# Optimization experiments

Measured on AMD Instinct MI355X. Metric: run time of the kernel, lower is better.

## Reference

```python
import jax, jax.numpy as jnp
import numpy as np

N = 100000   # nodes
E = 1600000  # edges
D_IN, D_H, D_OUT = 128, 128, 64
BN_EPS = 1e-5


def setup_inputs() -> dict:
    key = jax.random.key(0)
    ks = jax.random.split(key, 12)

    def lin_w(k, fan_in, shape):
        s = 1.0 / np.sqrt(fan_in)
        return jax.random.uniform(k, shape, jnp.float32, -s, s)

    return {
        "x": jax.random.normal(ks[0], (N, D_IN), jnp.float32),
        "edge_index": jax.random.randint(ks[1], (2, E), 0, N, dtype=jnp.int64),
        "edge_weight": jax.random.uniform(ks[2], (E,), jnp.float32),
        "W1": lin_w(ks[3], D_IN, (D_IN, D_H)),
        "b1": jnp.zeros((D_H,), jnp.float32),
        "W2": lin_w(ks[4], D_H, (D_H, D_H)),
        "b2": jnp.zeros((D_H,), jnp.float32),
        "W3": lin_w(ks[5], D_H, (D_H, D_OUT)),
        "b3": jnp.zeros((D_OUT,), jnp.float32),
        "gamma1": jnp.ones((D_H,), jnp.float32),
        "beta1": jnp.zeros((D_H,), jnp.float32),
        "gamma2": jnp.ones((D_H,), jnp.float32),
        "beta2": jnp.zeros((D_H,), jnp.float32),
    }


def _gcn_conv(x, src, dst, w, W, b):
    # PyG GCNConv: x' = D^{-1/2} (A + I) D^{-1/2} (x W) + b, self-loop weight 1
    n = x.shape[0]
    h = x @ W                                   # [N, d_out]
    loop = jnp.arange(n, dtype=src.dtype)
    s = jnp.concatenate([src, loop])            # [E+N]
    d = jnp.concatenate([dst, loop])
    ww = jnp.concatenate([w, jnp.ones((n,), w.dtype)])
    deg = jax.ops.segment_sum(ww, d, num_segments=n)          # in-degree at targets
    dinv = jnp.where(deg > 0, jax.lax.rsqrt(deg), 0.0)
    norm = dinv[s] * ww * dinv[d]               # [E+N]
    msg = h[s] * norm[:, None]                  # gather + scale
    out = jax.ops.segment_sum(msg, d, num_segments=n)
    return out + b


def _batch_norm(x, gamma, beta):
    mean = jnp.mean(x, axis=0)
    var = jnp.mean(jnp.square(x - mean), axis=0)  # biased, as BatchNorm uses
    return (x - mean) * jax.lax.rsqrt(var + BN_EPS) * gamma + beta


def reference(x, edge_index, edge_weight, W1, b1, W2, b2, W3, b3,
              gamma1, beta1, gamma2, beta2):
    src, dst = edge_index[0], edge_index[1]
    h = _gcn_conv(x, src, dst, edge_weight, W1, b1)
    h = jax.nn.relu(_batch_norm(h, gamma1, beta1))
    h = _gcn_conv(h, src, dst, edge_weight, W2, b2)
    h = jax.nn.relu(_batch_norm(h, gamma2, beta2))
    return _gcn_conv(h, src, dst, edge_weight, W3, b3)
```

## Files before the change

kernel.cpp:

```cpp
#include <hip/hip_runtime.h>
#include <hip/hip_fp16.h>
#include <cstdint>
#include <cstddef>

#define BN_EPS 1e-5f
#define KB 256
#define BSH 9

typedef _Float16 half8 __attribute__((ext_vector_type(8)));
typedef float floatx4 __attribute__((ext_vector_type(4)));

__device__ __forceinline__ float loadS(const __half* p) { return __half2float(*p); }
__device__ __forceinline__ float2 load2(const __half* p) {
    return __half22float2(*(const __half2*)p);
}
__device__ __forceinline__ void storeS(float* p, float v) { *p = v; }
__device__ __forceinline__ void storeS(__half* p, float v) { *p = __float2half(v); }
__device__ __forceinline__ void store2(float* p, float a, float b) {
    *(float2*)p = make_float2(a, b);
}
__device__ __forceinline__ void store2(__half* p, float a, float b) {
    *(__half2*)p = __floats2half2_rn(a, b);
}
__device__ __forceinline__ float wn_of(unsigned v) {
    __half_raw hr; hr.x = (unsigned short)(v & 0x7fffu);
    return __half2float((__half)hr);
}

static __device__ __forceinline__ int load_edge(const void* ei, int mode64, long long pos) {
    if (mode64) return (int)((const long long*)ei)[pos];
    return ((const int*)ei)[pos];
}

__device__ __forceinline__ int detect_mode64(const unsigned* eiw) {
    const int lane = (int)threadIdx.x & 63;
    unsigned m = 0;
    for (int i = lane; i < 2048; i += 64) m |= eiw[2 * i + 1];
    return (__ballot(m != 0) == 0ULL) ? 1 : 0;
}

__global__ __launch_bounds__(256) void init_hist_kernel(const void* __restrict__ ei,
                                                        unsigned* __restrict__ tk,
                                                        unsigned* __restrict__ pc, int E, int epb,
                                                        const float* __restrict__ W1,
                                                        const float* __restrict__ W2,
                                                        const float* __restrict__ W3,
                                                        _Float16* __restrict__ WT1,
                                                        _Float16* __restrict__ WT2,
                                                        _Float16* __restrict__ WT3) {
    const int bid = (int)blockIdx.x;
    const int tid = (int)threadIdx.x;
    if (bid < 160) {
        if (bid == 0 && tid < 8) tk[tid] = 0u;
        const int t_ = bid;
        if (t_ < 64) {
            int t = t_ * 256 + tid;
            int n = t / 128, k = t % 128;
            WT1[t] = (_Float16)W1[k * 128 + n];
        } else if (t_ < 128) {
            int t = (t_ - 64) * 256 + tid;
            int n = t / 128, k = t % 128;
            WT2[t] = (_Float16)W2[k * 128 + n];
        } else {
            int t = (t_ - 128) * 256 + tid;
            int n = t / 128, k = t % 128;
            WT3[t] = (_Float16)W3[k * 64 + n];
        }
        return;
    }
    __shared__ unsigned h[256];
    const int k = bid - 160;
    h[tid] = 0;
    __syncthreads();
    const int md = detect_mode64((const unsigned*)ei);
    const int e0 = k * epb;
    const int e1 = min(E, e0 + epb);
    for (int e = e0 + tid; e < e1; e += 256) {
        int d = load_edge(ei, md, (long long)E + e);
        atomicAdd(&h[d >> BSH], 1u);
    }
    __syncthreads();
    pc[k * 256 + tid] = h[tid];
}

__global__ __launch_bounds__(256) void scan_pc_kernel(unsigned* __restrict__ pc,
                                                      int* __restrict__ tb,
                                                      int* __restrict__ bbase,
                                                      float* __restrict__ gsum,
                                                      float* __restrict__ gsq,
                                                      unsigned* __restrict__ tk, int nbuck) {
    __shared__ int red[256];
    __shared__ int lastFlag;
    const int b = (int)blockIdx.x;
    const int tid = (int)threadIdx.x;
    const unsigned v = pc[tid * 256 + b];
    red[tid] = (int)v;
    __syncthreads();
    for (int off = 1; off < 256; off <<= 1) {
        int t = 0;
        if (tid >= off) t = red[tid - off];
        __syncthreads();
        red[tid] += t;
        __syncthreads();
    }
    pc[tid * 256 + b] = (unsigned)(red[tid] - (int)v);
    if (tid == 255)
        __hip_atomic_store(&tb[b], red[255], __ATOMIC_RELEASE, __HIP_MEMORY_SCOPE_AGENT);
    __syncthreads();
    if (tid == 0) {
        unsigned t = __hip_atomic_fetch_add(tk, 1u, __ATOMIC_ACQ_REL, __HIP_MEMORY_SCOPE_AGENT);
        lastFlag = (t == (unsigned)gridDim.x - 1u) ? 1 : 0;
    }
    __syncthreads();
    if (!lastFlag) return;
    const int v2 = (tid < nbuck)
        ? __hip_atomic_load(&tb[tid], __ATOMIC_ACQUIRE, __HIP_MEMORY_SCOPE_AGENT) : 0;
    __syncthreads();
    red[tid] = v2;
    __syncthreads();
    for (int off = 1; off < 256; off <<= 1) {
        int t = 0;
        if (tid >= off) t = red[tid - off];
        __syncthreads();
        red[tid] += t;
        __syncthreads();
    }
    bbase[tid] = red[tid] - v2;
    if (tid < 128) { gsum[tid] = 0.0f; gsq[tid] = 0.0f; }
}

template <int M, bool BN, typename TI, bool SCALE>
__device__ __forceinline__ void gemm_body(int gbid, const TI* __restrict__ X,
                                          const _Float16* __restrict__ WTg,
                                          const float* __restrict__ sc,
                                          const float* __restrict__ sh,
                                          const float* __restrict__ dinvp,
                                          __half* __restrict__ Hout, int N,
                                          _Float16* WT ) {
    constexpr int CT = M / 16;
    constexpr int LDK = 136;

    for (int t = threadIdx.x; t < M * 16; t += 256) {
        int n = t / 16, seg = t % 16;
        *(half8*)&WT[n * LDK + seg * 8] = *(const half8*)&WTg[n * 128 + seg * 8];
    }
    __syncthreads();

    const int wave = (int)threadIdx.x >> 6;
    const int lane = (int)threadIdx.x & 63;
    const int qd = lane >> 4;
    const int ln = lane & 15;
    const int tile0 = gbid * 64 + wave * 16;
    int ar = tile0 + ln;
    if (ar >= N) ar = N - 1;

    half8 aF[4];
    const TI* xr = X + (size_t)ar * 128 + qd * 8;
#pragma unroll
    for (int kb = 0; kb < 4; ++kb) {
        float vv[8];
        if constexpr (sizeof(TI) == 4) {
            float4 v0 = *(const float4*)(xr + kb * 32);
            float4 v1 = *(const float4*)(xr + kb * 32 + 4);
            vv[0] = v0.x; vv[1] = v0.y; vv[2] = v0.z; vv[3] = v0.w;
            vv[4] = v1.x; vv[5] = v1.y; vv[6] = v1.z; vv[7] = v1.w;
        } else {
            half8 raw = *(const half8*)(xr + kb * 32);
#pragma unroll
            for (int j = 0; j < 8; ++j) vv[j] = (float)raw[j];
        }
        if (BN) {
            const int kbase = kb * 32 + qd * 8;
#pragma unroll
            for (int j = 0; j < 8; ++j)
                vv[j] = fmaxf(fmaf(vv[j], sc[kbase + j], sh[kbase + j]), 0.0f);
        }
        half8 a;
#pragma unroll
        for (int j = 0; j < 8; ++j) a[j] = (_Float16)vv[j];
        aF[kb] = a;
    }

    float dvr[4];
    if constexpr (SCALE) {
#pragma unroll
        for (int r = 0; r < 4; ++r) {
            int orow = tile0 + qd * 4 + r;
            dvr[r] = (orow < N) ? dinvp[orow] : 1.0f;
        }
    }

#pragma unroll
    for (int ct = 0; ct < CT; ++ct) {
        floatx4 acc = {0.0f, 0.0f, 0.0f, 0.0f};
#pragma unroll
        for (int kb = 0; kb < 4; ++kb) {
            half8 b = *(const half8*)&WT[(ct * 16 + ln) * LDK + kb * 32 + qd * 8];
            acc = __builtin_amdgcn_mfma_f32_16x16x32_f16(aF[kb], b, acc, 0, 0, 0);
        }
#pragma unroll
        for (int r = 0; r < 4; ++r) {
            int orow = tile0 + qd * 4 + r;
            if (orow < N) {
                float o = acc[r];
                if constexpr (SCALE) o *= dvr[r];
                Hout[(size_t)orow * M + ct * 16 + ln] = __float2half(o);
            }
        }
    }
}

__global__ __launch_bounds__(256) void sort_gemm1_kernel(const void* __restrict__ ei,
                                                         const float* __restrict__ ew,
                                                         const unsigned* __restrict__ pc,
                                                         const int* __restrict__ bbase,
                                                         unsigned long long* __restrict__ sortedE,
                                                         int E, int epb, int GB,
                                                         const float* __restrict__ X,
                                                         const _Float16* __restrict__ WT1g,
                                                         __half* __restrict__ Hout, int N) {
    __shared__ _Float16 WT[128 * 136];
    __shared__ unsigned off_s[256];
    if ((int)blockIdx.x < GB) {
        gemm_body<128, false, float, false>(blockIdx.x, X, WT1g, nullptr, nullptr, nullptr,
                                            Hout, N, WT);
        return;
    }
    const int k = (int)blockIdx.x - GB;
    const int tid = (int)threadIdx.x;
    off_s[tid] = (unsigned)bbase[tid] + pc[k * 256 + tid];
    __syncthreads();
    const int md = detect_mode64((const unsigned*)ei);
    const int e0 = k * epb;
    const int e1 = min(E, e0 + epb);
    for (int e = e0 + tid; e < e1; e += 256) {
        int d = load_edge(ei, md, (long long)E + e);
        int s = load_edge(ei, md, e);
        float wv = ew[e];
        unsigned slot = atomicAdd(&off_s[d >> BSH], 1u);
        sortedE[slot] = ((unsigned long long)(unsigned)d << 33) |
                        ((unsigned long long)(unsigned)s << 16) |
                        (unsigned long long)(unsigned short)__half_as_ushort(__float2half(wv));
    }
}

__global__ __launch_bounds__(256) void csr_build_kernel(const unsigned long long* __restrict__ sortedE,
                                                        const int* __restrict__ bbase,
                                                        const int* __restrict__ tb,
                                                        float* __restrict__ dinv,
                                                        int* __restrict__ cnt,
                                                        int* __restrict__ row_start,
                                                        unsigned* __restrict__ edata,
                                                        __half* __restrict__ H, int N) {
    __shared__ unsigned cs[512];
    __shared__ float ws[512];
    __shared__ float dv[512];
    __shared__ unsigned sc[512];
    __shared__ unsigned cur[512];
    __shared__ int red[256];
    const int b = (int)blockIdx.x;
    const int tid = (int)threadIdx.x;
    const int n0 = b << BSH;
    const int base = bbase[b];
    const int len = tb[b];

    cs[tid] = 0; cs[tid + 256] = 0;
    ws[tid] = 0.0f; ws[tid + 256] = 0.0f;
    cur[tid] = 0; cur[tid + 256] = 0;
    __syncthreads();

    for (int i = tid; i < len; i += 256) {
        unsigned long long p = sortedE[base + i];
        unsigned fine = (unsigned)(p >> 33) - (unsigned)n0;
        atomicAdd(&cs[fine], 1u);
        __half_raw hr; hr.x = (unsigned short)(p & 0xFFFFu);
        atomicAdd(&ws[fine], __half2float((__half)hr));
    }
    __syncthreads();

    const unsigned a0 = cs[2 * tid];
    const unsigned a1 = cs[2 * tid + 1];
    const int s2 = (int)(a0 + a1);
    red[tid] = s2;
    __syncthreads();
    for (int off = 1; off < 256; off <<= 1) {
        int t = 0;
        if (tid >= off) t = red[tid - off];
        __syncthreads();
        red[tid] += t;
        __syncthreads();
    }
    const int excl2 = red[tid] - s2;
    sc[2 * tid] = (unsigned)excl2;
    sc[2 * tid + 1] = (unsigned)(excl2 + (int)a0);

#pragma unroll
    for (int q = 0; q < 2; ++q) {
        const int f = tid + q * 256;
        const int node = n0 + f;
        const float dvv = rsqrtf(1.0f + ws[f]);
        dv[f] = dvv;
        if (node < N) {
            dinv[node] = dvv;
            cnt[node] = (int)cs[f];
            row_start[node] = base + (int)sc[f];
        }
    }
    __syncthreads();

    for (int i = tid; i < len; i += 256) {
        unsigned long long p = sortedE[base + i];
        unsigned fine = (unsigned)(p >> 33) - (unsigned)n0;
        unsigned s = (unsigned)(p >> 16) & 0x1FFFFu;
        __half_raw hr; hr.x = (unsigned short)(p & 0xFFFFu);
        float wnp = __half2float((__half)hr) * dv[fine];
        unsigned r = atomicAdd(&cur[fine], 1u);
        unsigned hb = (unsigned)__half_as_ushort(__float2half(wnp)) & 0x7fffu;
        edata[base + (int)sc[fine] + (int)r] = (s << 15) | hb;
    }

    for (int idx = tid; idx < (1 << BSH) * 16; idx += 256) {
        const int r = idx >> 4;
        const int node = n0 + r;
        if (node < N) {
            const int seg = idx & 15;
            _Float16* hp = (_Float16*)H + (size_t)node * 128 + seg * 8;
            half8 h = *(half8*)hp;
            const float dvv = dv[r];
#pragma unroll
            for (int j = 0; j < 8; ++j) h[j] = (_Float16)((float)h[j] * dvv);
            *(half8*)hp = h;
        }
    }
}

template <int D, bool BIAS, typename TY>
__global__ __launch_bounds__(256) void agg_kernel(const __half* __restrict__ H,
                                                  const unsigned* __restrict__ edata,
                                                  const int* __restrict__ row_start,
                                                  const int* __restrict__ cnt,
                                                  const float* __restrict__ dinv,
                                                  const float* __restrict__ bias,
                                                  TY* __restrict__ Y, int N) {
    constexpr int VPT = D / 64;
    const int lane = (int)threadIdx.x & 63;
    const int i = (int)blockIdx.x * 4 + ((int)threadIdx.x >> 6);
    if (i >= N) return;
    const int c0 = lane * VPT;
    const float di = dinv[i];

    float acc0, acc1 = 0.0f;
    if constexpr (VPT == 2) {
        float2 h = load2(H + (size_t)i * D + c0);
        acc0 = di * h.x;
        acc1 = di * h.y;
    } else {
        acc0 = di * loadS(H + (size_t)i * D + c0);
    }

    const int base = row_start[i];
    const int n = cnt[i];
    for (int off = 0; off < n; off += 64) {
        const int rem = n - off;
        unsigned ev = 0;
        if (lane < rem) ev = edata[base + off + lane];
        const int mm = min(64, rem);
        for (int j = 0; j < mm; j += 8) {
            const unsigned e0 = __shfl(ev, j),     e1 = __shfl(ev, j + 1);
            const unsigned e2 = __shfl(ev, j + 2), e3 = __shfl(ev, j + 3);
            const unsigned e4 = __shfl(ev, j + 4), e5 = __shfl(ev, j + 5);
            const unsigned e6 = __shfl(ev, j + 6), e7 = __shfl(ev, j + 7);
            const float w0 = wn_of(e0), w1 = wn_of(e1), w2 = wn_of(e2), w3 = wn_of(e3);
            const float w4 = wn_of(e4), w5 = wn_of(e5), w6 = wn_of(e6), w7 = wn_of(e7);
            if constexpr (VPT == 2) {
                float2 h0 = load2(H + (size_t)(e0 >> 15) * D + c0);
                float2 h1 = load2(H + (size_t)(e1 >> 15) * D + c0);
                float2 h2 = load2(H + (size_t)(e2 >> 15) * D + c0);
                float2 h3 = load2(H + (size_t)(e3 >> 15) * D + c0);
                float2 h4 = load2(H + (size_t)(e4 >> 15) * D + c0);
                float2 h5 = load2(H + (size_t)(e5 >> 15) * D + c0);
                float2 h6 = load2(H + (size_t)(e6 >> 15) * D + c0);
                float2 h7 = load2(H + (size_t)(e7 >> 15) * D + c0);
                acc0 = fmaf(w0, h0.x, acc0); acc1 = fmaf(w0, h0.y, acc1);
                acc0 = fmaf(w1, h1.x, acc0); acc1 = fmaf(w1, h1.y, acc1);
                acc0 = fmaf(w2, h2.x, acc0); acc1 = fmaf(w2, h2.y, acc1);
                acc0 = fmaf(w3, h3.x, acc0); acc1 = fmaf(w3, h3.y, acc1);
                acc0 = fmaf(w4, h4.x, acc0); acc1 = fmaf(w4, h4.y, acc1);
                acc0 = fmaf(w5, h5.x, acc0); acc1 = fmaf(w5, h5.y, acc1);
                acc0 = fmaf(w6, h6.x, acc0); acc1 = fmaf(w6, h6.y, acc1);
                acc0 = fmaf(w7, h7.x, acc0); acc1 = fmaf(w7, h7.y, acc1);
            } else {
                float h0 = loadS(H + (size_t)(e0 >> 15) * D + c0);
                float h1 = loadS(H + (size_t)(e1 >> 15) * D + c0);
                float h2 = loadS(H + (size_t)(e2 >> 15) * D + c0);
                float h3 = loadS(H + (size_t)(e3 >> 15) * D + c0);
                float h4 = loadS(H + (size_t)(e4 >> 15) * D + c0);
                float h5 = loadS(H + (size_t)(e5 >> 15) * D + c0);
                float h6 = loadS(H + (size_t)(e6 >> 15) * D + c0);
                float h7 = loadS(H + (size_t)(e7 >> 15) * D + c0);
                acc0 = fmaf(w0, h0, acc0);
                acc0 = fmaf(w1, h1, acc0);
                acc0 = fmaf(w2, h2, acc0);
                acc0 = fmaf(w3, h3, acc0);
                acc0 = fmaf(w4, h4, acc0);
                acc0 = fmaf(w5, h5, acc0);
                acc0 = fmaf(w6, h6, acc0);
                acc0 = fmaf(w7, h7, acc0);
            }
        }
    }

    if constexpr (VPT == 2) {
        if (BIAS) { acc0 += bias[c0]; acc1 += bias[c0 + 1]; }
        store2(Y + (size_t)i * D + c0, acc0, acc1);
    } else {
        if (BIAS) acc0 += bias[c0];
        storeS(Y + (size_t)i * D + c0, acc0);
    }
}

template <int M, bool BN, typename TI, bool ZERO, bool SCALE>
__global__ __launch_bounds__(256) void gemm_mfma_kernel(const TI* __restrict__ X,
                                                        const _Float16* __restrict__ WTg,
                                                        const float* __restrict__ sc,
                                                        const float* __restrict__ sh,
                                                        const float* __restrict__ dinvp,
                                                        __half* __restrict__ Hout, int N,
                                                        float* __restrict__ gsum,
                                                        float* __restrict__ gsq, int GB) {
    __shared__ _Float16 WT[M * 136];
    if (ZERO && (int)blockIdx.x == GB) {
        if (threadIdx.x < 128) { gsum[threadIdx.x] = 0.0f; gsq[threadIdx.x] = 0.0f; }
        return;
    }
    gemm_body<M, BN, TI, SCALE>(blockIdx.x, X, WTg, sc, sh, dinvp, Hout, N, WT);
}

__global__ __launch_bounds__(256) void stats_kernel(const __half* __restrict__ Y,
                                                    float* __restrict__ gsum,
                                                    float* __restrict__ gsq,
                                                    unsigned* __restrict__ tk,
                                                    const float* __restrict__ gamma,
                                                    const float* __restrict__ beta,
                                                    float* __restrict__ sc,
                                                    float* __restrict__ sh, int N) {
    __shared__ float ls[256], lq[256];
    __shared__ int lastFlag;
    const int tid = (int)threadIdx.x;
    const int c = tid & 127;
    const int half_ = tid >> 7;
    float s = 0.0f, q = 0.0f;
    for (int row = (int)blockIdx.x * 2 + half_; row < N; row += 512) {
        float v = __half2float(Y[(size_t)row * 128 + c]);
        s += v;
        q = fmaf(v, v, q);
    }
    ls[tid] = s; lq[tid] = q;
    __syncthreads();
    if (tid < 128) {
        atomicAdd(&gsum[c], ls[tid] + ls[tid + 128]);
        atomicAdd(&gsq[c],  lq[tid] + lq[tid + 128]);
    }
    __syncthreads();
    if (tid == 0) {
        unsigned t = __hip_atomic_fetch_add(tk, 1u, __ATOMIC_ACQ_REL, __HIP_MEMORY_SCOPE_AGENT);
        lastFlag = (t == (unsigned)gridDim.x - 1u) ? 1 : 0;
    }
    __syncthreads();
    if (!lastFlag) return;
    if (tid < 128) {
        float gs = __hip_atomic_load(&gsum[tid], __ATOMIC_ACQUIRE, __HIP_MEMORY_SCOPE_AGENT);
        float gq = __hip_atomic_load(&gsq[tid], __ATOMIC_ACQUIRE, __HIP_MEMORY_SCOPE_AGENT);
        float inv_n = 1.0f / (float)N;
        float mean = gs * inv_n;
        float var = gq * inv_n - mean * mean;
        float scale = gamma[tid] * rsqrtf(var + BN_EPS);
        sc[tid] = scale;
        sh[tid] = beta[tid] - mean * scale;
    }
}

extern "C" void kernel_launch(void* const* d_in, const int* in_sizes, int n_in,
                              void* d_out, int out_size, void* d_ws, size_t ws_size,
                              hipStream_t stream) {
    const float* x   = (const float*)d_in[0];
    const void*  ei  = d_in[1];
    const float* ew  = (const float*)d_in[2];
    const float* W1  = (const float*)d_in[3];
    const float* W2  = (const float*)d_in[5];
    const float* W3  = (const float*)d_in[7];
    const float* b3  = (const float*)d_in[8];
    const float* g1  = (const float*)d_in[9];
    const float* be1 = (const float*)d_in[10];
    const float* g2  = (const float*)d_in[11];
    const float* be2 = (const float*)d_in[12];
    float* out = (float*)d_out;

    const int N = in_sizes[0] / 128;
    const int E = in_sizes[2];

    char* w = (char*)d_ws;
    size_t off = 0;
    auto alloc = [&](size_t bytes) -> void* {
        void* p = w + off;
        off += (bytes + 255) & ~(size_t)255;
        return p;
    };
    unsigned* pc     = (unsigned*)alloc(256 * 256 * 4);
    int*   tb        = (int*)  alloc(256 * 4);
    int*   bbase     = (int*)  alloc(256 * 4);
    unsigned long long* sortedE = (unsigned long long*)alloc((size_t)E * 8);
    float* dinv      = (float*)alloc((size_t)N * 4);
    int*   cnt       = (int*)  alloc((size_t)N * 4);
    int*   row_start = (int*)  alloc((size_t)N * 4);
    unsigned* edata  = (unsigned*)alloc((size_t)E * 4);
    unsigned* tk     = (unsigned*)alloc(256);
    float* gsum      = (float*)alloc(128 * 4);
    float* gsq       = (float*)alloc(128 * 4);
    float* scb       = (float*)alloc(128 * 4);
    float* shb       = (float*)alloc(128 * 4);
    _Float16* WT1    = (_Float16*)alloc(128 * 128 * 2);
    _Float16* WT2    = (_Float16*)alloc(128 * 128 * 2);
    _Float16* WT3    = (_Float16*)alloc(128 * 64 * 2);
    __half* H        = (__half*)alloc((size_t)N * 128 * 2);
    __half* Yh       = (__half*)alloc((size_t)N * 128 * 2);
    (void)ws_size; (void)n_in; (void)out_size;

    const int epb   = (E + KB - 1) / KB;
    const int nbuck = (N + (1 << BSH) - 1) >> BSH;
    const int gb    = (N + 63) / 64;
    const int ab    = (N + 3) / 4;

    init_hist_kernel<<<160 + KB, 256, 0, stream>>>(ei, tk, pc, E, epb,
                                                   W1, W2, W3, WT1, WT2, WT3);
    scan_pc_kernel<<<nbuck, 256, 0, stream>>>(pc, tb, bbase, gsum, gsq, &tk[0], nbuck);
    sort_gemm1_kernel<<<gb + KB, 256, 0, stream>>>(ei, ew, pc, bbase, sortedE, E,
                                                   epb, gb, x, WT1, H, N);
    csr_build_kernel<<<nbuck, 256, 0, stream>>>(sortedE, bbase, tb, dinv, cnt, row_start,
                                                edata, H, N);

    agg_kernel<128, false, __half><<<ab, 256, 0, stream>>>(H, edata, row_start, cnt, dinv, nullptr, Yh, N);
    stats_kernel<<<256, 256, 0, stream>>>(Yh, gsum, gsq, &tk[1], g1, be1, scb, shb, N);

    gemm_mfma_kernel<128, true, __half, true, true><<<gb + 1, 256, 0, stream>>>(
        Yh, WT2, scb, shb, dinv, H, N, gsum, gsq, gb);
    agg_kernel<128, false, __half><<<ab, 256, 0, stream>>>(H, edata, row_start, cnt, dinv, nullptr, Yh, N);
    stats_kernel<<<256, 256, 0, stream>>>(Yh, gsum, gsq, &tk[2], g2, be2, scb, shb, N);

    gemm_mfma_kernel<64, true, __half, false, true><<<gb, 256, 0, stream>>>(
        Yh, WT3, scb, shb, dinv, H, N, nullptr, nullptr, gb);
    agg_kernel<64, true, float><<<ab, 256, 0, stream>>>(H, edata, row_start, cnt, dinv, b3, out, N);
}
```

Measured before the change: 513.2 us.

## Move source-side dinv scaling into aggregation and raise sort block count

Removes the pre-scaling of H rows by dinv from the GEMM epilogues and from the H rescale pass in csr_build. Instead, the aggregation kernel multiplies each edge weight by dinv of the source node, and the self term by dinv squared. This eliminates a read-modify-write pass over H and lets the GEMM1 blocks run independently of the CSR build. The costs are an extra random gather of dinv per edge in every aggregation and a larger count of histogram/sort blocks (KB from 256 to 1024), with the scan now summing four partitions per thread. The sort blocks are also reordered ahead of the GEMM blocks in the fused launch.

```diff
diff --git a/kernel.cpp b/kernel.cpp
--- a/kernel.cpp
+++ b/kernel.cpp
@@ -4,7 +4,7 @@
 #include <cstddef>
 
 #define BN_EPS 1e-5f
-#define KB 256
+#define KB 1024
 #define BSH 9
 
 typedef _Float16 half8 __attribute__((ext_vector_type(8)));
@@ -93,8 +93,16 @@
     __shared__ int lastFlag;
     const int b = (int)blockIdx.x;
     const int tid = (int)threadIdx.x;
-    const unsigned v = pc[tid * 256 + b];
-    red[tid] = (int)v;
+    unsigned v[4];
+    int vals[4];
+    int s = 0;
+#pragma unroll
+    for (int j = 0; j < 4; ++j) {
+        v[j] = pc[(tid * 4 + j) * 256 + b];
+        vals[j] = s;
+        s += (int)v[j];
+    }
+    red[tid] = s;
     __syncthreads();
     for (int off = 1; off < 256; off <<= 1) {
         int t = 0;
@@ -103,7 +111,10 @@
         red[tid] += t;
         __syncthreads();
     }
-    pc[tid * 256 + b] = (unsigned)(red[tid] - (int)v);
+    const int excl = red[tid] - s;
+#pragma unroll
+    for (int j = 0; j < 4; ++j)
+        pc[(tid * 4 + j) * 256 + b] = (unsigned)(excl + vals[j]);
     if (tid == 255)
         __hip_atomic_store(&tb[b], red[255], __ATOMIC_RELEASE, __HIP_MEMORY_SCOPE_AGENT);
     __syncthreads();
@@ -129,12 +140,11 @@
     if (tid < 128) { gsum[tid] = 0.0f; gsq[tid] = 0.0f; }
 }
 
-template <int M, bool BN, typename TI, bool SCALE>
+template <int M, bool BN, typename TI>
 __device__ __forceinline__ void gemm_body(int gbid, const TI* __restrict__ X,
                                           const _Float16* __restrict__ WTg,
                                           const float* __restrict__ sc,
                                           const float* __restrict__ sh,
-                                          const float* __restrict__ dinvp,
                                           __half* __restrict__ Hout, int N,
                                           _Float16* WT ) {
     constexpr int CT = M / 16;
@@ -181,15 +191,6 @@
         aF[kb] = a;
     }
 
-    float dvr[4];
-    if constexpr (SCALE) {
-#pragma unroll
-        for (int r = 0; r < 4; ++r) {
-            int orow = tile0 + qd * 4 + r;
-            dvr[r] = (orow < N) ? dinvp[orow] : 1.0f;
-        }
-    }
-
 #pragma unroll
     for (int ct = 0; ct < CT; ++ct) {
         floatx4 acc = {0.0f, 0.0f, 0.0f, 0.0f};
@@ -201,11 +202,7 @@
 #pragma unroll
         for (int r = 0; r < 4; ++r) {
             int orow = tile0 + qd * 4 + r;
-            if (orow < N) {
-                float o = acc[r];
-                if constexpr (SCALE) o *= dvr[r];
-                Hout[(size_t)orow * M + ct * 16 + ln] = __float2half(o);
-            }
+            if (orow < N) Hout[(size_t)orow * M + ct * 16 + ln] = __float2half(acc[r]);
         }
     }
 }
@@ -215,18 +212,18 @@
                                                          const unsigned* __restrict__ pc,
                                                          const int* __restrict__ bbase,
                                                          unsigned long long* __restrict__ sortedE,
-                                                         int E, int epb, int GB,
+                                                         int E, int epb,
                                                          const float* __restrict__ X,
                                                          const _Float16* __restrict__ WT1g,
                                                          __half* __restrict__ Hout, int N) {
     __shared__ _Float16 WT[128 * 136];
     __shared__ unsigned off_s[256];
-    if ((int)blockIdx.x < GB) {
-        gemm_body<128, false, float, false>(blockIdx.x, X, WT1g, nullptr, nullptr, nullptr,
-                                            Hout, N, WT);
+    if ((int)blockIdx.x >= KB) {
+        gemm_body<128, false, float>((int)blockIdx.x - KB, X, WT1g, nullptr, nullptr,
+                                     Hout, N, WT);
         return;
     }
-    const int k = (int)blockIdx.x - GB;
+    const int k = (int)blockIdx.x;
     const int tid = (int)threadIdx.x;
     off_s[tid] = (unsigned)bbase[tid] + pc[k * 256 + tid];
     __syncthreads();
@@ -250,8 +247,7 @@
                                                         float* __restrict__ dinv,
                                                         int* __restrict__ cnt,
                                                         int* __restrict__ row_start,
-                                                        unsigned* __restrict__ edata,
-                                                        __half* __restrict__ H, int N) {
+                                                        unsigned* __restrict__ edata, int N) {
     __shared__ unsigned cs[512];
     __shared__ float ws[512];
     __shared__ float dv[512];
@@ -317,20 +313,6 @@
         unsigned r = atomicAdd(&cur[fine], 1u);
         unsigned hb = (unsigned)__half_as_ushort(__float2half(wnp)) & 0x7fffu;
         edata[base + (int)sc[fine] + (int)r] = (s << 15) | hb;
-    }
-
-    for (int idx = tid; idx < (1 << BSH) * 16; idx += 256) {
-        const int r = idx >> 4;
-        const int node = n0 + r;
-        if (node < N) {
-            const int seg = idx & 15;
-            _Float16* hp = (_Float16*)H + (size_t)node * 128 + seg * 8;
-            half8 h = *(half8*)hp;
-            const float dvv = dv[r];
-#pragma unroll
-            for (int j = 0; j < 8; ++j) h[j] = (_Float16)((float)h[j] * dvv);
-            *(half8*)hp = h;
-        }
     }
 }
 
@@ -348,14 +330,15 @@
     if (i >= N) return;
     const int c0 = lane * VPT;
     const float di = dinv[i];
+    const float dii = di * di;
 
     float acc0, acc1 = 0.0f;
     if constexpr (VPT == 2) {
         float2 h = load2(H + (size_t)i * D + c0);
-        acc0 = di * h.x;
-        acc1 = di * h.y;
+        acc0 = dii * h.x;
+        acc1 = dii * h.y;
     } else {
-        acc0 = di * loadS(H + (size_t)i * D + c0);
+        acc0 = dii * loadS(H + (size_t)i * D + c0);
     }
 
     const int base = row_start[i];
@@ -370,8 +353,14 @@
             const unsigned e2 = __shfl(ev, j + 2), e3 = __shfl(ev, j + 3);
             const unsigned e4 = __shfl(ev, j + 4), e5 = __shfl(ev, j + 5);
             const unsigned e6 = __shfl(ev, j + 6), e7 = __shfl(ev, j + 7);
-            const float w0 = wn_of(e0), w1 = wn_of(e1), w2 = wn_of(e2), w3 = wn_of(e3);
-            const float w4 = wn_of(e4), w5 = wn_of(e5), w6 = wn_of(e6), w7 = wn_of(e7);
+            const float w0 = dinv[e0 >> 15] * wn_of(e0);
+            const float w1 = dinv[e1 >> 15] * wn_of(e1);
+            const float w2 = dinv[e2 >> 15] * wn_of(e2);
+            const float w3 = dinv[e3 >> 15] * wn_of(e3);
+            const float w4 = dinv[e4 >> 15] * wn_of(e4);
+            const float w5 = dinv[e5 >> 15] * wn_of(e5);
+            const float w6 = dinv[e6 >> 15] * wn_of(e6);
+            const float w7 = dinv[e7 >> 15] * wn_of(e7);
             if constexpr (VPT == 2) {
                 float2 h0 = load2(H + (size_t)(e0 >> 15) * D + c0);
                 float2 h1 = load2(H + (size_t)(e1 >> 15) * D + c0);
@@ -419,12 +408,11 @@
     }
 }
 
-template <int M, bool BN, typename TI, bool ZERO, bool SCALE>
+template <int M, bool BN, typename TI, bool ZERO>
 __global__ __launch_bounds__(256) void gemm_mfma_kernel(const TI* __restrict__ X,
                                                         const _Float16* __restrict__ WTg,
                                                         const float* __restrict__ sc,
                                                         const float* __restrict__ sh,
-                                                        const float* __restrict__ dinvp,
                                                         __half* __restrict__ Hout, int N,
                                                         float* __restrict__ gsum,
                                                         float* __restrict__ gsq, int GB) {
@@ -433,7 +421,7 @@
         if (threadIdx.x < 128) { gsum[threadIdx.x] = 0.0f; gsq[threadIdx.x] = 0.0f; }
         return;
     }
-    gemm_body<M, BN, TI, SCALE>(blockIdx.x, X, WTg, sc, sh, dinvp, Hout, N, WT);
+    gemm_body<M, BN, TI>(blockIdx.x, X, WTg, sc, sh, Hout, N, WT);
 }
 
 __global__ __launch_bounds__(256) void stats_kernel(const __half* __restrict__ Y,
@@ -506,7 +494,7 @@
         off += (bytes + 255) & ~(size_t)255;
         return p;
     };
-    unsigned* pc     = (unsigned*)alloc(256 * 256 * 4);
+    unsigned* pc     = (unsigned*)alloc((size_t)KB * 256 * 4);
     int*   tb        = (int*)  alloc(256 * 4);
     int*   bbase     = (int*)  alloc(256 * 4);
     unsigned long long* sortedE = (unsigned long long*)alloc((size_t)E * 8);
@@ -534,20 +522,20 @@
     init_hist_kernel<<<160 + KB, 256, 0, stream>>>(ei, tk, pc, E, epb,
                                                    W1, W2, W3, WT1, WT2, WT3);
     scan_pc_kernel<<<nbuck, 256, 0, stream>>>(pc, tb, bbase, gsum, gsq, &tk[0], nbuck);
-    sort_gemm1_kernel<<<gb + KB, 256, 0, stream>>>(ei, ew, pc, bbase, sortedE, E,
-                                                   epb, gb, x, WT1, H, N);
+    sort_gemm1_kernel<<<KB + gb, 256, 0, stream>>>(ei, ew, pc, bbase, sortedE, E,
+                                                   epb, x, WT1, H, N);
     csr_build_kernel<<<nbuck, 256, 0, stream>>>(sortedE, bbase, tb, dinv, cnt, row_start,
-                                                edata, H, N);
+                                                edata, N);
 
     agg_kernel<128, false, __half><<<ab, 256, 0, stream>>>(H, edata, row_start, cnt, dinv, nullptr, Yh, N);
     stats_kernel<<<256, 256, 0, stream>>>(Yh, gsum, gsq, &tk[1], g1, be1, scb, shb, N);
 
-    gemm_mfma_kernel<128, true, __half, true, true><<<gb + 1, 256, 0, stream>>>(
-        Yh, WT2, scb, shb, dinv, H, N, gsum, gsq, gb);
+    gemm_mfma_kernel<128, true, __half, true><<<gb + 1, 256, 0, stream>>>(
+        Yh, WT2, scb, shb, H, N, gsum, gsq, gb);
     agg_kernel<128, false, __half><<<ab, 256, 0, stream>>>(H, edata, row_start, cnt, dinv, nullptr, Yh, N);
     stats_kernel<<<256, 256, 0, stream>>>(Yh, gsum, gsq, &tk[2], g2, be2, scb, shb, N);
 
-    gemm_mfma_kernel<64, true, __half, false, true><<<gb, 256, 0, stream>>>(
-        Yh, WT3, scb, shb, dinv, H, N, nullptr, nullptr, gb);
+    gemm_mfma_kernel<64, true, __half, false><<<gb, 256, 0, stream>>>(
+        Yh, WT3, scb, shb, H, N, nullptr, nullptr, gb);
     agg_kernel<64, true, float><<<ab, 256, 0, stream>>>(H, edata, row_start, cnt, dinv, b3, out, N);
 }
```

Result: faster. 497.7 us (-3.0%).
